# Kernel optimization log

Hardware: AMD Instinct MI355X
Metric: run time of the kernel (lower is better)

Reference implementation:

```python
import jax, jax.numpy as jnp
import numpy as np

D_MODEL = 512
NUM_HEADS = 8
D_K = D_MODEL // NUM_HEADS  # 64
LN_EPS = 1e-5


def setup_inputs() -> dict:
    key = jax.random.key(0)
    ks = jax.random.split(key, 6)
    B, S, D = 8, 1024, D_MODEL
    scale = 1.0 / np.sqrt(D)
    return {
        "query": jax.random.normal(ks[0], (B, S, D), jnp.float32),
        "key": jax.random.normal(ks[1], (B, S, D), jnp.float32),
        "value": jax.random.normal(ks[2], (B, S, D), jnp.float32),
        "Wq": jax.random.normal(ks[3], (D, D), jnp.float32) * scale,
        "bq": jnp.zeros((D,), jnp.float32),
        "Wk": jax.random.normal(ks[4], (D, D), jnp.float32) * scale,
        "bk": jnp.zeros((D,), jnp.float32),
        "Wo": jax.random.normal(ks[5], (D, D * NUM_HEADS), jnp.float32) * (1.0 / np.sqrt(D * NUM_HEADS)),
        "bo": jnp.zeros((D,), jnp.float32),
        "gamma": jnp.ones((D,), jnp.float32),
        "beta": jnp.zeros((D,), jnp.float32),
    }


def reference(query, key, value, Wq, bq, Wk, bk, Wo, bo, gamma, beta):
    B, S, D = value.shape
    h, dk = NUM_HEADS, D_K
    # QK projections -> [B, h, S, dk]
    q = (query @ Wq.T + bq).reshape(B, S, h, dk).transpose(0, 2, 1, 3)
    k = (key @ Wk.T + bk).reshape(B, S, h, dk).transpose(0, 2, 1, 3)
    # scaled dot-product scores [B, h, Sq, Sk]
    scores = jnp.einsum("bhqd,bhkd->bhqk", q, k) / jnp.sqrt(jnp.asarray(dk, q.dtype))
    attn = jax.nn.softmax(scores, axis=-1)
    # value broadcast across heads: value is [B, Sk, D] -> per-head output [B, h, Sq, D]
    x = jnp.einsum("bhqk,bkd->bhqd", attn, value)
    # concat heads -> [B, Sq, h*D], output projection back to D
    x = x.transpose(0, 2, 1, 3).reshape(B, S, h * D)
    x = x @ Wo.T + bo
    # residual + LayerNorm (dropout = identity in eval)
    y = value + x
    mu = jnp.mean(y, axis=-1, keepdims=True)
    var = jnp.var(y, axis=-1, keepdims=True)
    out = (y - mu) * jax.lax.rsqrt(var + LN_EPS) * gamma + beta
    return out, attn
```

## Files before the change

### kernel.cpp

```cpp
#include <hip/hip_runtime.h>
#include <hip/hip_bf16.h>

#define B_ 8
#define S_ 1024
#define D_ 512
#define H_ 8
#define DK_ 64
#define HD_ 4096

typedef __attribute__((ext_vector_type(8))) short bf16x8;
typedef __attribute__((ext_vector_type(4))) float f32x4;

static __device__ __forceinline__ unsigned short f2bf(float f) {
    unsigned u = __float_as_uint(f);
    unsigned r = (u + 0x7fffu + ((u >> 16) & 1u)) >> 16;
    return (unsigned short)r;
}

static __device__ __forceinline__ void gload16(const unsigned short* g, unsigned short* l) {
    __builtin_amdgcn_global_load_lds(
        (const __attribute__((address_space(1))) void*)g,
        (__attribute__((address_space(3))) void*)l, 16, 0, 0);
}

static __device__ __forceinline__ int plidx(int ql, int k) {
    return ql * 1024 + ((((k >> 3) ^ (ql & 7))) << 3) + (k & 7);
}

__global__ __launch_bounds__(256) void cvt_kernel(
    const float* __restrict__ src, unsigned short* __restrict__ dst)
{
    const size_t i = ((size_t)blockIdx.x * 256 + threadIdx.x) * 4;
    float4 v = *(const float4*)&src[i];
    ushort4 u = { f2bf(v.x), f2bf(v.y), f2bf(v.z), f2bf(v.w) };
    *(ushort4*)&dst[i] = u;
}

__global__ __launch_bounds__(256) void vt_kernel(
    const float* __restrict__ V, unsigned short* __restrict__ Vt)
{
    __shared__ float tile[32][33];
    const int b = blockIdx.z, s0 = blockIdx.x * 32, e0 = blockIdx.y * 32;
    const int t = threadIdx.x;
    const int r = t >> 3, c4 = (t & 7) * 4;
    float4 v = *(const float4*)&V[((size_t)b * S_ + s0 + r) * D_ + e0 + c4];
    tile[r][c4 + 0] = v.x; tile[r][c4 + 1] = v.y;
    tile[r][c4 + 2] = v.z; tile[r][c4 + 3] = v.w;
    __syncthreads();
    ushort4 u;
    u.x = f2bf(tile[c4 + 0][r]); u.y = f2bf(tile[c4 + 1][r]);
    u.z = f2bf(tile[c4 + 2][r]); u.w = f2bf(tile[c4 + 3][r]);
    *(ushort4*)&Vt[((size_t)b * D_ + e0 + r) * S_ + s0 + c4] = u;
}

template<int KDIM, int MODE>
__global__ __launch_bounds__(256) void gemm128(
    const unsigned short* __restrict__ A, const unsigned short* __restrict__ Bw,
    const float* __restrict__ bias, const float* __restrict__ Vres,
    void* __restrict__ Out, float scale)
{
    const int o = blockIdx.x;
    const int nb = (o & 7) * 32 + (o >> 3);
    const int m0 = (nb >> 2) * 128;
    const int n0 = (nb & 3) * 128;

    __shared__ __align__(16) unsigned short As[2][128 * 32];
    __shared__ __align__(16) unsigned short Bs[2][128 * 32];

    const int t = threadIdx.x;
    const int wave = t >> 6, lane = t & 63;
    const int wr = wave >> 1, wc = wave & 1;
    const int lr = lane & 15, g = lane >> 4;
    const int gx = (g ^ (lr & 3)) << 3;

    f32x4 acc[4][4];
    #pragma unroll
    for (int r = 0; r < 4; ++r)
        #pragma unroll
        for (int c = 0; c < 4; ++c) acc[r][c] = (f32x4){0.f, 0.f, 0.f, 0.f};

    const int sub = lane >> 2;
    const int cb  = (((lane & 3) ^ (sub & 3)) << 3);

    auto stage = [&](int buf, int k0) {
        #pragma unroll
        for (int s = 0; s < 2; ++s) {
            const int chunk = s * 4 + wave;
            const int row = chunk * 16 + sub;
            gload16(&A [(size_t)(m0 + row) * KDIM + k0 + cb], &As[buf][chunk * 512]);
            gload16(&Bw[(size_t)(n0 + row) * KDIM + k0 + cb], &Bs[buf][chunk * 512]);
        }
    };
    auto compute = [&](int cur) {
        bf16x8 af[4], bfr[4];
        #pragma unroll
        for (int r = 0; r < 4; ++r)
            af[r] = *(const bf16x8*)&As[cur][(wr * 64 + r * 16 + lr) * 32 + gx];
        #pragma unroll
        for (int c = 0; c < 4; ++c)
            bfr[c] = *(const bf16x8*)&Bs[cur][(wc * 64 + c * 16 + lr) * 32 + gx];
        #pragma unroll
        for (int c = 0; c < 4; ++c)
            #pragma unroll
            for (int r = 0; r < 4; ++r)
                acc[r][c] = __builtin_amdgcn_mfma_f32_16x16x32_bf16(af[r], bfr[c], acc[r][c], 0, 0, 0);
    };

    const int NT = KDIM / 32;
    stage(0, 0);
    __syncthreads();
    int cur = 0;
    for (int tt = 0; tt < NT - 1; ++tt) {
        stage(cur ^ 1, (tt + 1) * 32);
        compute(cur);
        __syncthreads();
        cur ^= 1;
    }
    compute(cur);

    float bn[4];
    #pragma unroll
    for (int c = 0; c < 4; ++c) bn[c] = bias[n0 + wc * 64 + c * 16 + lr];

    #pragma unroll
    for (int r = 0; r < 4; ++r) {
        #pragma unroll
        for (int c = 0; c < 4; ++c) {
            const int n = n0 + wc * 64 + c * 16 + lr;
            #pragma unroll
            for (int i = 0; i < 4; ++i) {
                const int m = m0 + wr * 64 + r * 16 + g * 4 + i;
                if constexpr (MODE == 0) {
                    const int srow = m & 1023, bb = m >> 10;
                    const int h = n >> 6, dk = n & 63;
                    ((unsigned short*)Out)[(((size_t)(bb * H_ + h)) * S_ + srow) * DK_ + dk] =
                        f2bf((acc[r][c][i] + bn[c]) * scale);
                } else {
                    const size_t oo = (size_t)m * D_ + n;
                    ((float*)Out)[oo] = acc[r][c][i] + bn[c] + Vres[oo];
                }
            }
        }
    }
}

__global__ __launch_bounds__(1024, 4) void fused_attn(
    const unsigned short* __restrict__ Qbf,
    const unsigned short* __restrict__ Kbf,
    const unsigned short* __restrict__ Vt,
    float* __restrict__ attn,
    unsigned short* __restrict__ AV)
{
    const int bh = blockIdx.y;
    const int b = bh >> 3, h = bh & 7;
    const int q0 = blockIdx.x * 64;
    const unsigned short* Qb = Qbf + (size_t)bh * S_ * DK_;
    const unsigned short* Kb = Kbf + (size_t)bh * S_ * DK_;
    const unsigned short* Vb = Vt + (size_t)b * D_ * S_;
    float* outp = attn + ((size_t)bh << 20);

    __shared__ unsigned short PL[64 * 1024];
    __shared__ float redm[64][16];
    __shared__ float rowm[64];

    const int t = threadIdx.x;
    const int wave = t >> 6, lane = t & 63;
    const int wcol = wave * 64;
    const int lr = lane & 15;
    const int g  = lane >> 4;

    f32x4 acc[4][4];
    #pragma unroll
    for (int r = 0; r < 4; ++r)
        #pragma unroll
        for (int c = 0; c < 4; ++c) acc[r][c] = (f32x4){0.f, 0.f, 0.f, 0.f};

    #pragma unroll
    for (int kk = 0; kk < 2; ++kk) {
        bf16x8 af[4];
        #pragma unroll
        for (int r = 0; r < 4; ++r)
            af[r] = *(const bf16x8*)&Kb[(size_t)(wcol + r * 16 + lr) * DK_ + kk * 32 + g * 8];
        bf16x8 qf[4];
        #pragma unroll
        for (int c = 0; c < 4; ++c)
            qf[c] = *(const bf16x8*)&Qb[(size_t)(q0 + c * 16 + lr) * DK_ + kk * 32 + g * 8];
        #pragma unroll
        for (int r = 0; r < 4; ++r)
            #pragma unroll
            for (int c = 0; c < 4; ++c)
                acc[r][c] = __builtin_amdgcn_mfma_f32_16x16x32_bf16(af[r], qf[c], acc[r][c], 0, 0, 0);
    }

    float mloc[4];
    #pragma unroll
    for (int c = 0; c < 4; ++c) {
        float m = acc[0][c][0];
        #pragma unroll
        for (int r = 0; r < 4; ++r)
            #pragma unroll
            for (int i = 0; i < 4; ++i) m = fmaxf(m, acc[r][c][i]);
        m = fmaxf(m, __shfl_xor(m, 16));
        m = fmaxf(m, __shfl_xor(m, 32));
        mloc[c] = m;
    }
    if (lane < 16) {
        #pragma unroll
        for (int c = 0; c < 4; ++c) redm[c * 16 + lane][wave] = mloc[c];
    }
    __syncthreads();
    if (t < 64) {
        float m = redm[t][0];
        #pragma unroll
        for (int w = 1; w < 16; ++w) m = fmaxf(m, redm[t][w]);
        rowm[t] = m;
    }
    __syncthreads();
    float sloc[4];
    #pragma unroll
    for (int c = 0; c < 4; ++c) {
        const float m = rowm[c * 16 + lr];
        float s = 0.f;
        #pragma unroll
        for (int r = 0; r < 4; ++r)
            #pragma unroll
            for (int i = 0; i < 4; ++i) {
                float p = __expf(acc[r][c][i] - m);
                acc[r][c][i] = p;
                s += p;
            }
        s += __shfl_xor(s, 16);
        s += __shfl_xor(s, 32);
        sloc[c] = s;
    }
    if (lane < 16) {
        #pragma unroll
        for (int c = 0; c < 4; ++c) redm[c * 16 + lane][wave] = sloc[c];
    }
    __syncthreads();
    if (t < 64) {
        float s = redm[t][0];
        #pragma unroll
        for (int w = 1; w < 16; ++w) s += redm[t][w];
        rowm[t] = 1.0f / s;
    }
    __syncthreads();

    #pragma unroll
    for (int c = 0; c < 4; ++c) {
        const int ql = c * 16 + lr;
        const float ri = rowm[ql];
        #pragma unroll
        for (int r = 0; r < 4; ++r) {
            f32x4 v = acc[r][c];
            v[0] *= ri; v[1] *= ri; v[2] *= ri; v[3] *= ri;
            const int k = wcol + r * 16 + g * 4;
            unsigned p01 = (unsigned)f2bf(v[0]) | ((unsigned)f2bf(v[1]) << 16);
            unsigned p23 = (unsigned)f2bf(v[2]) | ((unsigned)f2bf(v[3]) << 16);
            uint2 pk = { p01, p23 };
            *(uint2*)&PL[plidx(ql, k)] = pk;
        }
    }
    __syncthreads();

    const int we = wave * 32;
    f32x4 accv[4][2];
    #pragma unroll
    for (int r = 0; r < 4; ++r)
        #pragma unroll
        for (int c = 0; c < 2; ++c) accv[r][c] = (f32x4){0.f, 0.f, 0.f, 0.f};

    for (int k0 = 0; k0 < S_; k0 += 32) {
        bf16x8 pa[4];
        #pragma unroll
        for (int r = 0; r < 4; ++r)
            pa[r] = *(const bf16x8*)&PL[plidx(r * 16 + lr, k0 + g * 8)];
        #pragma unroll
        for (int c = 0; c < 2; ++c) {
            const int e = we + c * 16 + lr;
            bf16x8 vf = *(const bf16x8*)&Vb[(size_t)e * S_ + k0 + g * 8];
            #pragma unroll
            for (int r = 0; r < 4; ++r)
                accv[r][c] = __builtin_amdgcn_mfma_f32_16x16x32_bf16(pa[r], vf, accv[r][c], 0, 0, 0);
        }
    }

    {
        const int arow = t >> 4;
        const int akb  = (t & 15) * 8;
        float* rowp = outp + ((size_t)(q0 + arow) << 10);
        #pragma unroll
        for (int j = 0; j < 8; ++j) {
            const int k = akb + j * 128;
            uint4 u = *(const uint4*)&PL[plidx(arow, k)];
            float4 f0, f1;
            f0.x = __uint_as_float((u.x & 0xffffu) << 16);
            f0.y = __uint_as_float(u.x & 0xffff0000u);
            f0.z = __uint_as_float((u.y & 0xffffu) << 16);
            f0.w = __uint_as_float(u.y & 0xffff0000u);
            f1.x = __uint_as_float((u.z & 0xffffu) << 16);
            f1.y = __uint_as_float(u.z & 0xffff0000u);
            f1.z = __uint_as_float((u.w & 0xffffu) << 16);
            f1.w = __uint_as_float(u.w & 0xffff0000u);
            *(float4*)&rowp[k] = f0;
            *(float4*)&rowp[k + 4] = f1;
        }
    }
    __syncthreads();

    unsigned short* PLs = PL;
    #pragma unroll
    for (int r = 0; r < 4; ++r)
        #pragma unroll
        for (int c = 0; c < 2; ++c) {
            const int e = we + c * 16 + lr;
            #pragma unroll
            for (int i = 0; i < 4; ++i) {
                const int q = r * 16 + g * 4 + i;
                PLs[q * 512 + (e ^ ((q & 7) << 3))] = f2bf(accv[r][c][i]);
            }
        }
    __syncthreads();
    {
        const int row = t >> 4;
        unsigned short* avp = AV + ((size_t)(b * S_ + q0 + row)) * HD_ + h * D_;
        #pragma unroll
        for (int j = 0; j < 4; ++j) {
            const int e0 = (t & 15) * 8 + j * 128;
            uint4 u = *(const uint4*)&PLs[row * 512 + (e0 ^ ((row & 7) << 3))];
            *(uint4*)&avp[e0] = u;
        }
    }
}

__global__ __launch_bounds__(256) void ln_kernel(
    float* __restrict__ Y, const float* __restrict__ gamma,
    const float* __restrict__ beta)
{
    const int lane = threadIdx.x & 63;
    const int wave = threadIdx.x >> 6;
    const size_t row = (size_t)blockIdx.x * 4 + wave;
    float* p = Y + row * D_;
    float4 v0 = *(float4*)&p[lane * 4];
    float4 v1 = *(float4*)&p[256 + lane * 4];
    float s = v0.x + v0.y + v0.z + v0.w + v1.x + v1.y + v1.z + v1.w;
    float q = v0.x * v0.x + v0.y * v0.y + v0.z * v0.z + v0.w * v0.w +
              v1.x * v1.x + v1.y * v1.y + v1.z * v1.z + v1.w * v1.w;
    #pragma unroll
    for (int m = 1; m < 64; m <<= 1) {
        s += __shfl_xor(s, m);
        q += __shfl_xor(q, m);
    }
    const float mu  = s * (1.f / 512.f);
    const float var = q * (1.f / 512.f) - mu * mu;
    const float r = rsqrtf(var + 1e-5f);
    const float4 g0 = *(const float4*)&gamma[lane * 4];
    const float4 g1 = *(const float4*)&gamma[256 + lane * 4];
    const float4 b0 = *(const float4*)&beta[lane * 4];
    const float4 b1 = *(const float4*)&beta[256 + lane * 4];
    v0.x = (v0.x - mu) * r * g0.x + b0.x;
    v0.y = (v0.y - mu) * r * g0.y + b0.y;
    v0.z = (v0.z - mu) * r * g0.z + b0.z;
    v0.w = (v0.w - mu) * r * g0.w + b0.w;
    v1.x = (v1.x - mu) * r * g1.x + b1.x;
    v1.y = (v1.y - mu) * r * g1.y + b1.y;
    v1.z = (v1.z - mu) * r * g1.z + b1.z;
    v1.w = (v1.w - mu) * r * g1.w + b1.w;
    *(float4*)&p[lane * 4] = v0;
    *(float4*)&p[256 + lane * 4] = v1;
}

extern "C" void kernel_launch(void* const* d_in, const int* in_sizes, int n_in,
                              void* d_out, int out_size, void* d_ws, size_t ws_size,
                              hipStream_t stream)
{
    const float* query = (const float*)d_in[0];
    const float* key   = (const float*)d_in[1];
    const float* value = (const float*)d_in[2];
    const float* Wq    = (const float*)d_in[3];
    const float* bq    = (const float*)d_in[4];
    const float* Wk    = (const float*)d_in[5];
    const float* bk    = (const float*)d_in[6];
    const float* Wo    = (const float*)d_in[7];
    const float* bo    = (const float*)d_in[8];
    const float* gamma = (const float*)d_in[9];
    const float* beta  = (const float*)d_in[10];

    float* out  = (float*)d_out;
    float* attn = out + (size_t)B_ * S_ * D_;
    char*  attnB = (char*)attn;

    char* ws = (char*)d_ws;
    unsigned short* AV   = (unsigned short*)ws;
    unsigned short* Vt   = (unsigned short*)(ws + ((size_t)64 << 20));
    unsigned short* Wobf = (unsigned short*)(ws + ((size_t)72 << 20));
    unsigned short* Qbf  = (unsigned short*)d_out;
    unsigned short* Kbf  = (unsigned short*)d_out + ((size_t)4 << 20);
    unsigned short* Xq   = (unsigned short*)(attnB + ((size_t)200 << 20));
    unsigned short* Xk   = (unsigned short*)(attnB + ((size_t)210 << 20));
    unsigned short* Wqbf = (unsigned short*)(attnB + ((size_t)220 << 20));
    unsigned short* Wkbf = (unsigned short*)(attnB + ((size_t)221 << 20));

    cvt_kernel<<<4096, 256, 0, stream>>>(query, Xq);
    cvt_kernel<<<4096, 256, 0, stream>>>(key,   Xk);
    cvt_kernel<<<256,  256, 0, stream>>>(Wq, Wqbf);
    cvt_kernel<<<256,  256, 0, stream>>>(Wk, Wkbf);
    cvt_kernel<<<2048, 256, 0, stream>>>(Wo, Wobf);
    vt_kernel<<<dim3(32, 16, 8), 256, 0, stream>>>(value, Vt);
    gemm128<512, 0><<<256, 256, 0, stream>>>(Xq, Wqbf, bq, nullptr, (void*)Qbf, 0.125f);
    gemm128<512, 0><<<256, 256, 0, stream>>>(Xk, Wkbf, bk, nullptr, (void*)Kbf, 1.0f);
    fused_attn<<<dim3(16, 64), 1024, 0, stream>>>(Qbf, Kbf, Vt, attn, AV);
    gemm128<4096, 1><<<256, 256, 0, stream>>>(AV, Wobf, bo, value, (void*)out, 0.f);
    ln_kernel<<<2048, 256, 0, stream>>>(out, gamma, beta);
}
```

Baseline: 396.6 us.

## Retile GEMMs, reorder attention P·V, add setprio and merged conversions

Several changes at once. Pairs of fp32-to-bf16 conversion launches are merged into one kernel each. The GEMMs are templated on a 64-wide N tile, so twice as many blocks run, and they use an XCD-aware block swizzle. The attention kernel remaps blocks across XCDs and writes the attn probabilities with nontemporal stores before the P·V product, so the store traffic overlaps with MFMA work. The V fragments are software-prefetched one step ahead, and AV is written directly from registers instead of being staged through LDS. MFMA sections are wrapped in s_setprio. An extra barrier is added before the redm reuse, which closes a possible race but adds a sync.

Result: faster. 349.1 us (-12.0%).

```diff
diff --git a/kernel.cpp b/kernel.cpp
--- a/kernel.cpp
+++ b/kernel.cpp
@@ -34,6 +34,20 @@
     float4 v = *(const float4*)&src[i];
     ushort4 u = { f2bf(v.x), f2bf(v.y), f2bf(v.z), f2bf(v.w) };
     *(ushort4*)&dst[i] = u;
+}
+
+__global__ __launch_bounds__(256) void cvt2_kernel(
+    const float* __restrict__ s0, unsigned short* __restrict__ d0,
+    const float* __restrict__ s1, unsigned short* __restrict__ d1, int nb0)
+{
+    const bool first = (int)blockIdx.x < nb0;
+    const float* s = first ? s0 : s1;
+    unsigned short* d = first ? d0 : d1;
+    const int bid = first ? blockIdx.x : blockIdx.x - nb0;
+    const size_t i = ((size_t)bid * 256 + threadIdx.x) * 4;
+    float4 v = *(const float4*)&s[i];
+    ushort4 u = { f2bf(v.x), f2bf(v.y), f2bf(v.z), f2bf(v.w) };
+    *(ushort4*)&d[i] = u;
 }
 
 __global__ __launch_bounds__(256) void vt_kernel(
@@ -53,19 +67,22 @@
     *(ushort4*)&Vt[((size_t)b * D_ + e0 + r) * S_ + s0 + c4] = u;
 }
 
-template<int KDIM, int MODE>
-__global__ __launch_bounds__(256) void gemm128(
+template<int KDIM, int TN, int MODE>
+__global__ __launch_bounds__(256) void gemm_t(
     const unsigned short* __restrict__ A, const unsigned short* __restrict__ Bw,
     const float* __restrict__ bias, const float* __restrict__ Vres,
     void* __restrict__ Out, float scale)
 {
+    constexpr int NB = 512 / TN;
+    constexpr int CF = TN / 32;
     const int o = blockIdx.x;
-    const int nb = (o & 7) * 32 + (o >> 3);
-    const int m0 = (nb >> 2) * 128;
-    const int n0 = (nb & 3) * 128;
+    const int cpx = gridDim.x / 8;
+    const int nb = (o % 8) * cpx + o / 8;
+    const int m0 = (nb / NB) * 128;
+    const int n0 = (nb % NB) * TN;
 
     __shared__ __align__(16) unsigned short As[2][128 * 32];
-    __shared__ __align__(16) unsigned short Bs[2][128 * 32];
+    __shared__ __align__(16) unsigned short Bs[2][TN * 32];
 
     const int t = threadIdx.x;
     const int wave = t >> 6, lane = t & 63;
@@ -73,11 +90,11 @@
     const int lr = lane & 15, g = lane >> 4;
     const int gx = (g ^ (lr & 3)) << 3;
 
-    f32x4 acc[4][4];
+    f32x4 acc[4][CF];
     #pragma unroll
     for (int r = 0; r < 4; ++r)
         #pragma unroll
-        for (int c = 0; c < 4; ++c) acc[r][c] = (f32x4){0.f, 0.f, 0.f, 0.f};
+        for (int c = 0; c < CF; ++c) acc[r][c] = (f32x4){0.f, 0.f, 0.f, 0.f};
 
     const int sub = lane >> 2;
     const int cb  = (((lane & 3) ^ (sub & 3)) << 3);
@@ -87,23 +104,30 @@
         for (int s = 0; s < 2; ++s) {
             const int chunk = s * 4 + wave;
             const int row = chunk * 16 + sub;
-            gload16(&A [(size_t)(m0 + row) * KDIM + k0 + cb], &As[buf][chunk * 512]);
+            gload16(&A[(size_t)(m0 + row) * KDIM + k0 + cb], &As[buf][chunk * 512]);
+        }
+        #pragma unroll
+        for (int s = 0; s < TN / 64; ++s) {
+            const int chunk = s * 4 + wave;
+            const int row = chunk * 16 + sub;
             gload16(&Bw[(size_t)(n0 + row) * KDIM + k0 + cb], &Bs[buf][chunk * 512]);
         }
     };
     auto compute = [&](int cur) {
-        bf16x8 af[4], bfr[4];
+        bf16x8 af[4], bfr[CF];
         #pragma unroll
         for (int r = 0; r < 4; ++r)
             af[r] = *(const bf16x8*)&As[cur][(wr * 64 + r * 16 + lr) * 32 + gx];
         #pragma unroll
-        for (int c = 0; c < 4; ++c)
-            bfr[c] = *(const bf16x8*)&Bs[cur][(wc * 64 + c * 16 + lr) * 32 + gx];
-        #pragma unroll
-        for (int c = 0; c < 4; ++c)
+        for (int c = 0; c < CF; ++c)
+            bfr[c] = *(const bf16x8*)&Bs[cur][(wc * (TN / 2) + c * 16 + lr) * 32 + gx];
+        __builtin_amdgcn_s_setprio(1);
+        #pragma unroll
+        for (int c = 0; c < CF; ++c)
             #pragma unroll
             for (int r = 0; r < 4; ++r)
                 acc[r][c] = __builtin_amdgcn_mfma_f32_16x16x32_bf16(af[r], bfr[c], acc[r][c], 0, 0, 0);
+        __builtin_amdgcn_s_setprio(0);
     };
 
     const int NT = KDIM / 32;
@@ -118,15 +142,15 @@
     }
     compute(cur);
 
-    float bn[4];
-    #pragma unroll
-    for (int c = 0; c < 4; ++c) bn[c] = bias[n0 + wc * 64 + c * 16 + lr];
+    float bn[CF];
+    #pragma unroll
+    for (int c = 0; c < CF; ++c) bn[c] = bias[n0 + wc * (TN / 2) + c * 16 + lr];
 
     #pragma unroll
     for (int r = 0; r < 4; ++r) {
         #pragma unroll
-        for (int c = 0; c < 4; ++c) {
-            const int n = n0 + wc * 64 + c * 16 + lr;
+        for (int c = 0; c < CF; ++c) {
+            const int n = n0 + wc * (TN / 2) + c * 16 + lr;
             #pragma unroll
             for (int i = 0; i < 4; ++i) {
                 const int m = m0 + wr * 64 + r * 16 + g * 4 + i;
@@ -151,9 +175,11 @@
     float* __restrict__ attn,
     unsigned short* __restrict__ AV)
 {
-    const int bh = blockIdx.y;
+    const int o = blockIdx.x;
+    const int nb = (o & 7) * 128 + (o >> 3);
+    const int bh = nb >> 4;
+    const int q0 = (nb & 15) * 64;
     const int b = bh >> 3, h = bh & 7;
-    const int q0 = blockIdx.x * 64;
     const unsigned short* Qb = Qbf + (size_t)bh * S_ * DK_;
     const unsigned short* Kb = Kbf + (size_t)bh * S_ * DK_;
     const unsigned short* Vb = Vt + (size_t)b * D_ * S_;
@@ -185,11 +211,13 @@
         #pragma unroll
         for (int c = 0; c < 4; ++c)
             qf[c] = *(const bf16x8*)&Qb[(size_t)(q0 + c * 16 + lr) * DK_ + kk * 32 + g * 8];
+        __builtin_amdgcn_s_setprio(1);
         #pragma unroll
         for (int r = 0; r < 4; ++r)
             #pragma unroll
             for (int c = 0; c < 4; ++c)
                 acc[r][c] = __builtin_amdgcn_mfma_f32_16x16x32_bf16(af[r], qf[c], acc[r][c], 0, 0, 0);
+        __builtin_amdgcn_s_setprio(0);
     }
 
     float mloc[4];
@@ -233,6 +261,7 @@
         s += __shfl_xor(s, 32);
         sloc[c] = s;
     }
+    __syncthreads();
     if (lane < 16) {
         #pragma unroll
         for (int c = 0; c < 4; ++c) redm[c * 16 + lane][wave] = sloc[c];
@@ -263,28 +292,6 @@
     }
     __syncthreads();
 
-    const int we = wave * 32;
-    f32x4 accv[4][2];
-    #pragma unroll
-    for (int r = 0; r < 4; ++r)
-        #pragma unroll
-        for (int c = 0; c < 2; ++c) accv[r][c] = (f32x4){0.f, 0.f, 0.f, 0.f};
-
-    for (int k0 = 0; k0 < S_; k0 += 32) {
-        bf16x8 pa[4];
-        #pragma unroll
-        for (int r = 0; r < 4; ++r)
-            pa[r] = *(const bf16x8*)&PL[plidx(r * 16 + lr, k0 + g * 8)];
-        #pragma unroll
-        for (int c = 0; c < 2; ++c) {
-            const int e = we + c * 16 + lr;
-            bf16x8 vf = *(const bf16x8*)&Vb[(size_t)e * S_ + k0 + g * 8];
-            #pragma unroll
-            for (int r = 0; r < 4; ++r)
-                accv[r][c] = __builtin_amdgcn_mfma_f32_16x16x32_bf16(pa[r], vf, accv[r][c], 0, 0, 0);
-        }
-    }
-
     {
         const int arow = t >> 4;
         const int akb  = (t & 15) * 8;
@@ -293,42 +300,64 @@
         for (int j = 0; j < 8; ++j) {
             const int k = akb + j * 128;
             uint4 u = *(const uint4*)&PL[plidx(arow, k)];
-            float4 f0, f1;
-            f0.x = __uint_as_float((u.x & 0xffffu) << 16);
-            f0.y = __uint_as_float(u.x & 0xffff0000u);
-            f0.z = __uint_as_float((u.y & 0xffffu) << 16);
-            f0.w = __uint_as_float(u.y & 0xffff0000u);
-            f1.x = __uint_as_float((u.z & 0xffffu) << 16);
-            f1.y = __uint_as_float(u.z & 0xffff0000u);
-            f1.z = __uint_as_float((u.w & 0xffffu) << 16);
-            f1.w = __uint_as_float(u.w & 0xffff0000u);
-            *(float4*)&rowp[k] = f0;
-            *(float4*)&rowp[k + 4] = f1;
-        }
-    }
-    __syncthreads();
-
-    unsigned short* PLs = PL;
+            f32x4 f0, f1;
+            f0[0] = __uint_as_float((u.x & 0xffffu) << 16);
+            f0[1] = __uint_as_float(u.x & 0xffff0000u);
+            f0[2] = __uint_as_float((u.y & 0xffffu) << 16);
+            f0[3] = __uint_as_float(u.y & 0xffff0000u);
+            f1[0] = __uint_as_float((u.z & 0xffffu) << 16);
+            f1[1] = __uint_as_float(u.z & 0xffff0000u);
+            f1[2] = __uint_as_float((u.w & 0xffffu) << 16);
+            f1[3] = __uint_as_float(u.w & 0xffff0000u);
+            __builtin_nontemporal_store(f0, (f32x4*)&rowp[k]);
+            __builtin_nontemporal_store(f1, (f32x4*)&rowp[k + 4]);
+        }
+    }
+
+    const int we = wave * 32;
+    f32x4 accv[4][2];
     #pragma unroll
     for (int r = 0; r < 4; ++r)
+        #pragma unroll
+        for (int c = 0; c < 2; ++c) accv[r][c] = (f32x4){0.f, 0.f, 0.f, 0.f};
+
+    const unsigned short* vp0 = Vb + (size_t)(we + lr) * S_ + g * 8;
+    const unsigned short* vp1 = Vb + (size_t)(we + 16 + lr) * S_ + g * 8;
+    bf16x8 vf0 = *(const bf16x8*)vp0;
+    bf16x8 vf1 = *(const bf16x8*)vp1;
+
+    for (int k0 = 0; k0 < S_; k0 += 32) {
+        bf16x8 nv0, nv1;
+        const int kn = k0 + 32;
+        if (kn < S_) {
+            nv0 = *(const bf16x8*)(vp0 + kn);
+            nv1 = *(const bf16x8*)(vp1 + kn);
+        }
+        bf16x8 pa[4];
+        #pragma unroll
+        for (int r = 0; r < 4; ++r)
+            pa[r] = *(const bf16x8*)&PL[plidx(r * 16 + lr, k0 + g * 8)];
+        __builtin_amdgcn_s_setprio(1);
+        #pragma unroll
+        for (int r = 0; r < 4; ++r)
+            accv[r][0] = __builtin_amdgcn_mfma_f32_16x16x32_bf16(pa[r], vf0, accv[r][0], 0, 0, 0);
+        #pragma unroll
+        for (int r = 0; r < 4; ++r)
+            accv[r][1] = __builtin_amdgcn_mfma_f32_16x16x32_bf16(pa[r], vf1, accv[r][1], 0, 0, 0);
+        __builtin_amdgcn_s_setprio(0);
+        if (kn < S_) { vf0 = nv0; vf1 = nv1; }
+    }
+
+    #pragma unroll
+    for (int r = 0; r < 4; ++r) {
         #pragma unroll
         for (int c = 0; c < 2; ++c) {
             const int e = we + c * 16 + lr;
             #pragma unroll
             for (int i = 0; i < 4; ++i) {
-                const int q = r * 16 + g * 4 + i;
-                PLs[q * 512 + (e ^ ((q & 7) << 3))] = f2bf(accv[r][c][i]);
+                const int row = q0 + r * 16 + g * 4 + i;
+                AV[((size_t)(b * S_ + row)) * HD_ + h * D_ + e] = f2bf(accv[r][c][i]);
             }
-        }
-    __syncthreads();
-    {
-        const int row = t >> 4;
-        unsigned short* avp = AV + ((size_t)(b * S_ + q0 + row)) * HD_ + h * D_;
-        #pragma unroll
-        for (int j = 0; j < 4; ++j) {
-            const int e0 = (t & 15) * 8 + j * 128;
-            uint4 u = *(const uint4*)&PLs[row * 512 + (e0 ^ ((row & 7) << 3))];
-            *(uint4*)&avp[e0] = u;
         }
     }
 }
@@ -401,15 +430,13 @@
     unsigned short* Wqbf = (unsigned short*)(attnB + ((size_t)220 << 20));
     unsigned short* Wkbf = (unsigned short*)(attnB + ((size_t)221 << 20));
 
-    cvt_kernel<<<4096, 256, 0, stream>>>(query, Xq);
-    cvt_kernel<<<4096, 256, 0, stream>>>(key,   Xk);
-    cvt_kernel<<<256,  256, 0, stream>>>(Wq, Wqbf);
-    cvt_kernel<<<256,  256, 0, stream>>>(Wk, Wkbf);
+    cvt2_kernel<<<8192, 256, 0, stream>>>(query, Xq, key, Xk, 4096);
+    cvt2_kernel<<<512,  256, 0, stream>>>(Wq, Wqbf, Wk, Wkbf, 256);
     cvt_kernel<<<2048, 256, 0, stream>>>(Wo, Wobf);
     vt_kernel<<<dim3(32, 16, 8), 256, 0, stream>>>(value, Vt);
-    gemm128<512, 0><<<256, 256, 0, stream>>>(Xq, Wqbf, bq, nullptr, (void*)Qbf, 0.125f);
-    gemm128<512, 0><<<256, 256, 0, stream>>>(Xk, Wkbf, bk, nullptr, (void*)Kbf, 1.0f);
-    fused_attn<<<dim3(16, 64), 1024, 0, stream>>>(Qbf, Kbf, Vt, attn, AV);
-    gemm128<4096, 1><<<256, 256, 0, stream>>>(AV, Wobf, bo, value, (void*)out, 0.f);
+    gemm_t<512, 64, 0><<<512, 256, 0, stream>>>(Xq, Wqbf, bq, nullptr, (void*)Qbf, 0.125f);
+    gemm_t<512, 64, 0><<<512, 256, 0, stream>>>(Xk, Wkbf, bk, nullptr, (void*)Kbf, 1.0f);
+    fused_attn<<<1024, 1024, 0, stream>>>(Qbf, Kbf, Vt, attn, AV);
+    gemm_t<4096, 64, 1><<<512, 256, 0, stream>>>(AV, Wobf, bo, value, (void*)out, 0.f);
     ln_kernel<<<2048, 256, 0, stream>>>(out, gamma, beta);
 }
```
